# Kernel tuning notes

Hardware: AMD Instinct MI355X
Metric: run time of the kernel (lower is better)

## Reference

```python
import jax, jax.numpy as jnp
import numpy as np

B, L, CIN, COUT, S, H = 8, 16384, 256, 256, 4, 4
D = COUT // H          # depth = 64
LS = L // S            # pooled seq len = 4096


def setup_inputs() -> dict:
    key = jax.random.key(0)
    ks = jax.random.split(key, 9)
    sc_in = 1.0 / np.sqrt(CIN)
    sc_out = 1.0 / np.sqrt(COUT)
    return {
        "x": jax.random.normal(ks[0], (B, L, CIN), jnp.float32),
        "Wa": jax.random.normal(ks[1], (CIN, COUT), jnp.float32) * sc_in,
        "ba": jax.random.normal(ks[2], (COUT,), jnp.float32) * sc_in,
        "Wb": jax.random.normal(ks[3], (CIN, COUT), jnp.float32) * sc_in,
        "bb": jax.random.normal(ks[4], (COUT,), jnp.float32) * sc_in,
        "Wc": jax.random.normal(ks[5], (CIN, COUT), jnp.float32) * sc_in,
        "bc": jax.random.normal(ks[6], (COUT,), jnp.float32) * sc_in,
        "Wo": jax.random.normal(ks[7], (COUT, COUT), jnp.float32) * sc_out,
        "bo": jax.random.normal(ks[8], (COUT,), jnp.float32) * sc_out,
    }


def reference(x, Wa, ba, Wb, bb, Wc, bc, Wo, bo):
    # x: [B, L, CIN]
    # MaxPool1d(S) along the sequence axis (module pools the transposed [B,C,L])
    xp = x.reshape(B, LS, S, CIN).max(axis=2)        # [B, LS, CIN]

    x_a = xp @ Wa + ba                               # [B, LS, COUT]
    x_b = xp @ Wb + bb                               # [B, LS, COUT]
    # pool2 with Z=1 is the identity

    # split heads -> [B, H, LS, D]
    a = x_a.reshape(B, LS, H, D).transpose(0, 2, 1, 3)
    b = x_b.reshape(B, LS, H, D).transpose(0, 2, 1, 3)

    a = a.transpose(0, 1, 3, 2)                      # [B, H, D, LS]
    a = jax.nn.softmax(a, axis=-1)

    # looped_matmul, vectorized: for slice d, roll along LS by d (torch.roll
    # shifts right: rolled[l] = a[(l - d) mod LS]) and subtract, then contract
    # with the matching depth column of b.
    d_idx = jnp.arange(D, dtype=jnp.int32)[:, None]              # [D, 1]
    l_idx = jnp.arange(LS, dtype=jnp.int32)[None, :]             # [1, LS]
    roll_idx = (l_idx - d_idx) % LS                              # [D, LS]
    a_roll = a[:, :, d_idx, roll_idx]                            # [B, H, D, LS]
    diff = a - a_roll                                            # [B, H, D, LS]
    x_ab = jnp.einsum("bhdl,bhld->bhd", diff, b)                 # [B, H, D]

    # toSeq branch: c * x_ab broadcast over full sequence
    c = x @ Wc + bc                                              # [B, L, COUT]
    c = c.reshape(B, L, H, D).transpose(0, 2, 1, 3)              # [B, H, L, D]
    d = c * x_ab[:, :, None, :]                                  # [B, H, L, D]

    # module's split/cat recombines features as [depth, head] interleave:
    # out_feat[d*H + h] = d[..., h, d]
    d = d.transpose(0, 2, 3, 1).reshape(B, L, COUT)              # [B, L, COUT]

    return d @ Wo + bo                                           # [B, L, COUT]
```

## Files before the change

kernel.cpp:

```cpp
#include <hip/hip_runtime.h>
#include <hip/hip_bf16.h>
#include <hip/hip_fp16.h>

#define B_    8
#define L_    16384
#define CIN_  256
#define COUT_ 256
#define LS_   4096
#define H_    4
#define D_    64

typedef _Float16 f16x8 __attribute__((ext_vector_type(8)));
typedef _Float16 f16x4 __attribute__((ext_vector_type(4)));
typedef float    f32x4 __attribute__((ext_vector_type(4)));

__global__ __launch_bounds__(256) void k1_pool(const float* __restrict__ x,
                                               _Float16* __restrict__ xp) {
    int idx = blockIdx.x * 256 + threadIdx.x;
    int c4  = idx & 63;
    int bp  = idx >> 6;
    int b   = bp >> 12;
    int lp  = bp & 4095;
    const float4* base = (const float4*)(x + ((size_t)(b * L_ + lp * 4)) * CIN_) + c4;
    float4 m = base[0];
    #pragma unroll
    for (int s = 1; s < 4; ++s) {
        float4 v = base[s * 64];
        m.x = fmaxf(m.x, v.x); m.y = fmaxf(m.y, v.y);
        m.z = fmaxf(m.z, v.z); m.w = fmaxf(m.w, v.w);
    }
    f16x4 h;
    h[0] = (_Float16)m.x; h[1] = (_Float16)m.y;
    h[2] = (_Float16)m.z; h[3] = (_Float16)m.w;
    *(f16x4*)(xp + (size_t)bp * CIN_ + c4 * 4) = h;
}

__global__ __launch_bounds__(256) void k1b_wcvt(const float* __restrict__ Wa,
                                                const float* __restrict__ Wb,
                                                _Float16* __restrict__ WabT) {
    int n = blockIdx.x;
    int k = threadIdx.x;
    const float* W = (n < 256) ? Wa : Wb;
    int nn = n & 255;
    WabT[(size_t)n * 256 + k] = (_Float16)W[(size_t)k * 256 + nn];
}

__global__ __launch_bounds__(256) void k2_gemm_ab(const _Float16* __restrict__ xp,
                                                  const _Float16* __restrict__ WabT,
                                                  float* __restrict__ xabT) {
    int rowtile = blockIdx.x;
    int nhalf   = blockIdx.y;
    int row0    = rowtile * 64;
    int wave = threadIdx.x >> 6;
    int lane = threadIdx.x & 63;
    int lr = lane & 15, lg = lane >> 4;
    int col0 = wave * 64;
    const _Float16* Bbase = WabT + (size_t)(nhalf * 256) * 256;

    f32x4 acc[4][4] = {};
    for (int kk = 0; kk < 256; kk += 32) {
        f16x8 af[4], bf[4];
        #pragma unroll
        for (int t = 0; t < 4; ++t)
            af[t] = *(const f16x8*)(xp + (size_t)(row0 + t * 16 + lr) * 256 + kk + lg * 8);
        #pragma unroll
        for (int t = 0; t < 4; ++t)
            bf[t] = *(const f16x8*)(Bbase + (size_t)(col0 + t * 16 + lr) * 256 + kk + lg * 8);
        #pragma unroll
        for (int rt = 0; rt < 4; ++rt)
            #pragma unroll
            for (int ct = 0; ct < 4; ++ct)
                acc[rt][ct] = __builtin_amdgcn_mfma_f32_16x16x32_f16(af[rt], bf[ct], acc[rt][ct], 0, 0, 0);
    }
    int b  = row0 >> 12;
    int l0 = row0 & 4095;
    #pragma unroll
    for (int rt = 0; rt < 4; ++rt)
        #pragma unroll
        for (int ct = 0; ct < 4; ++ct) {
            int colg  = nhalf * 256 + col0 + ct * 16 + lr;
            int lbase = l0 + rt * 16 + lg * 4;
            *(f32x4*)(xabT + ((size_t)b * 512 + colg) * 4096 + lbase) = acc[rt][ct];
        }
}

__global__ __launch_bounds__(256) void k3_softmax(const float* __restrict__ xabT,
                                                  float* __restrict__ s) {
    int bid = blockIdx.x;
    int b = bid >> 8, ch = bid & 255, d = ch & 63;
    const float* arow = xabT + ((size_t)b * 512 + ch) * 4096;
    const float* brow = xabT + ((size_t)b * 512 + 256 + ch) * 4096;
    int t = threadIdx.x;

    __shared__ float wm[4], wz[4], ww[4];

    float m = -INFINITY;
    for (int l = t; l < 4096; l += 256) m = fmaxf(m, arow[l]);
    #pragma unroll
    for (int off = 32; off; off >>= 1) m = fmaxf(m, __shfl_xor(m, off));
    if ((t & 63) == 0) wm[t >> 6] = m;
    __syncthreads();
    m = fmaxf(fmaxf(wm[0], wm[1]), fmaxf(wm[2], wm[3]));

    float Z = 0.f, W = 0.f;
    for (int l = t; l < 4096; l += 256) {
        float e = __expf(arow[l] - m);
        Z += e;
        W += e * (brow[l] - brow[(l + d) & 4095]);
    }
    #pragma unroll
    for (int off = 32; off; off >>= 1) {
        Z += __shfl_xor(Z, off);
        W += __shfl_xor(W, off);
    }
    if ((t & 63) == 0) { wz[t >> 6] = Z; ww[t >> 6] = W; }
    __syncthreads();
    if (t == 0) {
        float Zs = wz[0] + wz[1] + wz[2] + wz[3];
        float Ws = ww[0] + ww[1] + ww[2] + ww[3];
        s[bid] = Ws / Zs;
    }
}

__global__ __launch_bounds__(256) void k4_buildM(const float* __restrict__ Wc,
                                                 const float* __restrict__ bc,
                                                 const float* __restrict__ Wo,
                                                 const float* __restrict__ bo,
                                                 const float* __restrict__ s,
                                                 _Float16* __restrict__ MT,
                                                 float* __restrict__ v) {
    int b = blockIdx.x, it = blockIdx.y;
    int i0 = it * 16;
    int n  = threadIdx.x;

    __shared__ float wc[16][257];
    __shared__ float sl[256], bcl[256];
    sl[n]  = s[b * 256 + n];
    bcl[n] = bc[n];
    #pragma unroll
    for (int ii = 0; ii < 16; ++ii) wc[ii][n] = Wc[(size_t)(i0 + ii) * 256 + n];
    __syncthreads();

    float acc[16] = {};
    float accv = 0.f;
    for (int j = 0; j < 256; ++j) {
        int pj = ((j & 63) << 2) | (j >> 6);
        float wo  = Wo[(size_t)pj * 256 + n];
        float tmp = sl[j] * wo;
        #pragma unroll
        for (int ii = 0; ii < 16; ++ii) acc[ii] += wc[ii][j] * tmp;
        accv += bcl[j] * tmp;
    }
    #pragma unroll
    for (int ii = 0; ii < 16; ++ii)
        MT[((size_t)b * 256 + n) * 256 + i0 + ii] = (_Float16)acc[ii];
    if (it == 0) v[b * 256 + n] = accv + bo[n];
}

__global__ __launch_bounds__(256) void k5_main(const float* __restrict__ x,
                                               const _Float16* __restrict__ MT,
                                               const float* __restrict__ v,
                                               float* __restrict__ out) {
    int bid  = blockIdx.x;
    int b    = bid >> 8;
    int row0 = bid * 64;
    int wave = threadIdx.x >> 6, lane = threadIdx.x & 63;
    int lr = lane & 15, lg = lane >> 4;
    int col0 = wave * 64;
    const _Float16* Bb = MT + (size_t)b * 256 * 256;

    f32x4 acc[4][4] = {};
    for (int kk = 0; kk < 256; kk += 32) {
        f16x8 af[4], bf[4];
        #pragma unroll
        for (int t = 0; t < 4; ++t) {
            const float* ap = x + (size_t)(row0 + t * 16 + lr) * 256 + kk + lg * 8;
            float4 f0 = *(const float4*)ap;
            float4 f1 = *(const float4*)(ap + 4);
            f16x8 a;
            a[0] = (_Float16)f0.x; a[1] = (_Float16)f0.y;
            a[2] = (_Float16)f0.z; a[3] = (_Float16)f0.w;
            a[4] = (_Float16)f1.x; a[5] = (_Float16)f1.y;
            a[6] = (_Float16)f1.z; a[7] = (_Float16)f1.w;
            af[t] = a;
        }
        #pragma unroll
        for (int t = 0; t < 4; ++t)
            bf[t] = *(const f16x8*)(Bb + (size_t)(col0 + t * 16 + lr) * 256 + kk + lg * 8);
        #pragma unroll
        for (int rt = 0; rt < 4; ++rt)
            #pragma unroll
            for (int ct = 0; ct < 4; ++ct)
                acc[rt][ct] = __builtin_amdgcn_mfma_f32_16x16x32_f16(af[rt], bf[ct], acc[rt][ct], 0, 0, 0);
    }
    #pragma unroll
    for (int ct = 0; ct < 4; ++ct) {
        int n = col0 + ct * 16 + lr;
        float vb = v[b * 256 + n];
        #pragma unroll
        for (int rt = 0; rt < 4; ++rt) {
            int r = row0 + rt * 16 + lg * 4;
            float* o = out + (size_t)r * 256 + n;
            #pragma unroll
            for (int reg = 0; reg < 4; ++reg)
                o[(size_t)reg * 256] = acc[rt][ct][reg] + vb;
        }
    }
}

extern "C" void kernel_launch(void* const* d_in, const int* in_sizes, int n_in,
                              void* d_out, int out_size, void* d_ws, size_t ws_size,
                              hipStream_t stream) {
    const float* x  = (const float*)d_in[0];
    const float* Wa = (const float*)d_in[1];
    const float* Wb = (const float*)d_in[3];
    const float* Wc = (const float*)d_in[5];
    const float* bc = (const float*)d_in[6];
    const float* Wo = (const float*)d_in[7];
    const float* bo = (const float*)d_in[8];
    float* out = (float*)d_out;

    char* w = (char*)d_ws;
    _Float16* xp   = (_Float16*)w;  w += (size_t)32768 * 256 * 2;
    _Float16* WabT = (_Float16*)w;  w += (size_t)512 * 256 * 2;
    float*    s    = (float*)w;     w += (size_t)8 * 256 * 4;
    _Float16* MT   = (_Float16*)w;  w += (size_t)8 * 256 * 256 * 2;
    float*    vb   = (float*)w;     w += (size_t)8 * 256 * 4;

    float* xabT = out;

    k1_pool  <<<8192, 256, 0, stream>>>(x, xp);
    k1b_wcvt <<<512, 256, 0, stream>>>(Wa, Wb, WabT);
    k2_gemm_ab<<<dim3(512, 2), 256, 0, stream>>>(xp, WabT, xabT);
    k3_softmax<<<2048, 256, 0, stream>>>(xabT, s);
    k4_buildM <<<dim3(8, 16), 256, 0, stream>>>(Wc, bc, Wo, bo, s, MT, vb);
    k5_main   <<<2048, 256, 0, stream>>>(x, MT, vb, out);
}
```

Before: 515.3 us.

## Build fused Wc·diag(s)·Wo matrix with MFMA instead of scalar FMA loop

The per-batch fused weight M = Wc·diag(s)·Wo_perm was computed with a scalar FP32 triple loop in 128 blocks. It is now split into a small kernel that scales the permuted Wo by s (and computes the bias vector) into fp16, and an MFMA GEMM kernel that multiplies fp16 Wc by it. Wc is converted to fp16 in the existing weight-conversion kernel. This adds one launch, an extra fp16 intermediate, and fp16 rounding of the scaled Wo. k4a runs on only 8 blocks with strided Wo reads, and k4b runs on only 32 blocks.

```diff
diff --git a/kernel.cpp b/kernel.cpp
--- a/kernel.cpp
+++ b/kernel.cpp
@@ -37,12 +37,19 @@
 
 __global__ __launch_bounds__(256) void k1b_wcvt(const float* __restrict__ Wa,
                                                 const float* __restrict__ Wb,
-                                                _Float16* __restrict__ WabT) {
+                                                const float* __restrict__ Wc,
+                                                _Float16* __restrict__ WabT,
+                                                _Float16* __restrict__ Wc16) {
     int n = blockIdx.x;
     int k = threadIdx.x;
-    const float* W = (n < 256) ? Wa : Wb;
-    int nn = n & 255;
-    WabT[(size_t)n * 256 + k] = (_Float16)W[(size_t)k * 256 + nn];
+    if (n < 512) {
+        const float* W = (n < 256) ? Wa : Wb;
+        int nn = n & 255;
+        WabT[(size_t)n * 256 + k] = (_Float16)W[(size_t)k * 256 + nn];
+    } else {
+        int r = n - 512;
+        Wc16[(size_t)r * 256 + k] = (_Float16)Wc[(size_t)r * 256 + k];
+    }
 }
 
 __global__ __launch_bounds__(256) void k2_gemm_ab(const _Float16* __restrict__ xp,
@@ -122,39 +129,74 @@
     }
 }
 
-__global__ __launch_bounds__(256) void k4_buildM(const float* __restrict__ Wc,
+__global__ __launch_bounds__(256) void k4a_scale(const float* __restrict__ Wo,
                                                  const float* __restrict__ bc,
-                                                 const float* __restrict__ Wo,
                                                  const float* __restrict__ bo,
                                                  const float* __restrict__ s,
-                                                 _Float16* __restrict__ MT,
+                                                 _Float16* __restrict__ WoBs,
                                                  float* __restrict__ v) {
-    int b = blockIdx.x, it = blockIdx.y;
-    int i0 = it * 16;
-    int n  = threadIdx.x;
-
-    __shared__ float wc[16][257];
+    int b = blockIdx.x;
+    int n = threadIdx.x;
     __shared__ float sl[256], bcl[256];
     sl[n]  = s[b * 256 + n];
     bcl[n] = bc[n];
-    #pragma unroll
-    for (int ii = 0; ii < 16; ++ii) wc[ii][n] = Wc[(size_t)(i0 + ii) * 256 + n];
     __syncthreads();
 
-    float acc[16] = {};
     float accv = 0.f;
-    for (int j = 0; j < 256; ++j) {
-        int pj = ((j & 63) << 2) | (j >> 6);
-        float wo  = Wo[(size_t)pj * 256 + n];
-        float tmp = sl[j] * wo;
-        #pragma unroll
-        for (int ii = 0; ii < 16; ++ii) acc[ii] += wc[ii][j] * tmp;
-        accv += bcl[j] * tmp;
-    }
-    #pragma unroll
-    for (int ii = 0; ii < 16; ++ii)
-        MT[((size_t)b * 256 + n) * 256 + i0 + ii] = (_Float16)acc[ii];
-    if (it == 0) v[b * 256 + n] = accv + bo[n];
+    _Float16* dst = WoBs + ((size_t)(b * 256 + n)) * 256;
+    for (int j0 = 0; j0 < 256; j0 += 8) {
+        f16x8 pack;
+        #pragma unroll
+        for (int e = 0; e < 8; ++e) {
+            int j  = j0 + e;
+            int pj = ((j & 63) << 2) | (j >> 6);
+            float wo  = Wo[(size_t)pj * 256 + n];
+            float val = sl[j] * wo;
+            accv += bcl[j] * val;
+            pack[e] = (_Float16)val;
+        }
+        *(f16x8*)(dst + j0) = pack;
+    }
+    v[b * 256 + n] = accv + bo[n];
+}
+
+__global__ __launch_bounds__(256) void k4b_buildM(const _Float16* __restrict__ Wc16,
+                                                  const _Float16* __restrict__ WoBs,
+                                                  _Float16* __restrict__ MT) {
+    int b    = blockIdx.x;
+    int row0 = blockIdx.y * 64;
+    int wave = threadIdx.x >> 6, lane = threadIdx.x & 63;
+    int lr = lane & 15, lg = lane >> 4;
+    int col0 = wave * 64;
+    const _Float16* Bb = WoBs + (size_t)b * 256 * 256;
+
+    f32x4 acc[4][4] = {};
+    for (int kk = 0; kk < 256; kk += 32) {
+        f16x8 af[4], bf[4];
+        #pragma unroll
+        for (int t = 0; t < 4; ++t)
+            af[t] = *(const f16x8*)(Wc16 + (size_t)(row0 + t * 16 + lr) * 256 + kk + lg * 8);
+        #pragma unroll
+        for (int t = 0; t < 4; ++t)
+            bf[t] = *(const f16x8*)(Bb + (size_t)(col0 + t * 16 + lr) * 256 + kk + lg * 8);
+        #pragma unroll
+        for (int rt = 0; rt < 4; ++rt)
+            #pragma unroll
+            for (int ct = 0; ct < 4; ++ct)
+                acc[rt][ct] = __builtin_amdgcn_mfma_f32_16x16x32_f16(af[rt], bf[ct], acc[rt][ct], 0, 0, 0);
+    }
+    #pragma unroll
+    for (int ct = 0; ct < 4; ++ct) {
+        int n = col0 + ct * 16 + lr;
+        #pragma unroll
+        for (int rt = 0; rt < 4; ++rt) {
+            int i0 = row0 + rt * 16 + lg * 4;
+            f16x4 h;
+            h[0] = (_Float16)acc[rt][ct][0]; h[1] = (_Float16)acc[rt][ct][1];
+            h[2] = (_Float16)acc[rt][ct][2]; h[3] = (_Float16)acc[rt][ct][3];
+            *(f16x4*)(MT + ((size_t)(b * 256 + n)) * 256 + i0) = h;
+        }
+    }
 }
 
 __global__ __launch_bounds__(256) void k5_main(const float* __restrict__ x,
@@ -223,16 +265,19 @@
     char* w = (char*)d_ws;
     _Float16* xp   = (_Float16*)w;  w += (size_t)32768 * 256 * 2;
     _Float16* WabT = (_Float16*)w;  w += (size_t)512 * 256 * 2;
+    _Float16* Wc16 = (_Float16*)w;  w += (size_t)256 * 256 * 2;
     float*    s    = (float*)w;     w += (size_t)8 * 256 * 4;
+    _Float16* WoBs = (_Float16*)w;  w += (size_t)8 * 256 * 256 * 2;
     _Float16* MT   = (_Float16*)w;  w += (size_t)8 * 256 * 256 * 2;
     float*    vb   = (float*)w;     w += (size_t)8 * 256 * 4;
 
     float* xabT = out;
 
-    k1_pool  <<<8192, 256, 0, stream>>>(x, xp);
-    k1b_wcvt <<<512, 256, 0, stream>>>(Wa, Wb, WabT);
+    k1_pool   <<<8192, 256, 0, stream>>>(x, xp);
+    k1b_wcvt  <<<768, 256, 0, stream>>>(Wa, Wb, Wc, WabT, Wc16);
     k2_gemm_ab<<<dim3(512, 2), 256, 0, stream>>>(xp, WabT, xabT);
     k3_softmax<<<2048, 256, 0, stream>>>(xabT, s);
-    k4_buildM <<<dim3(8, 16), 256, 0, stream>>>(Wc, bc, Wo, bo, s, MT, vb);
+    k4a_scale <<<8, 256, 0, stream>>>(Wo, bc, bo, s, WoBs, vb);
+    k4b_buildM<<<dim3(8, 4), 256, 0, stream>>>(Wc16, WoBs, MT);
     k5_main   <<<2048, 256, 0, stream>>>(x, MT, vb, out);
 }
```

Result: faster. 426.2 us (-17.3%).
